# Optimization experiments

Measured on AMD Instinct MI355X. Metric: run time of the kernel, lower is better.

## Reference

```python
import jax, jax.numpy as jnp
import numpy as np
from jax import lax

B, T, D, H, W = 2, 8, 64, 64, 64
E, HID = 4, 256


def _layernorm(x, g, b, eps=1e-5):
    m = x.mean(-1, keepdims=True)
    v = ((x - m) ** 2).mean(-1, keepdims=True)
    return (x - m) / jnp.sqrt(v + eps) * g + b


def _pscan(A, X, axis):
    # linear recurrence h_t = A_t * h_{t-1} + X_t via associative scan
    def comb(l, r):
        a1, x1 = l
        a2, x2 = r
        return a2 * a1, a2 * x1 + x2
    return lax.associative_scan(comb, (A, X), axis=axis)[1]


def setup_inputs() -> dict:
    key = jax.random.key(0)
    ks = jax.random.split(key, 32)
    r = lambda i, shape, s=1.0: jax.random.normal(ks[i], shape, jnp.float32) * s
    D2 = 2 * D
    return {
        'x_re': r(0, (B, T, D, H, W)), 'x_im': r(1, (B, T, D, H, W)),
        'dt': jax.random.uniform(ks[2], (T,), jnp.float32, 0.5, 1.0),
        'ln_s_g': jnp.ones(D2), 'ln_s_b': jnp.zeros(D2),
        'conv_w': r(3, (3, 3, D2, D2), 0.03), 'conv_b': jnp.zeros(D2),
        'mom_w': r(4, (D2, D2), 0.08), 'mom_b': jnp.zeros(D2),
        'adv_w': jnp.full((1,), 0.1, jnp.float32),
        'enc_re': r(5, (D, D), 0.1), 'enc_im': r(6, (D, D), 0.1),
        'dec_re': r(7, (D, D), 0.1), 'dec_im': r(8, (D, D), 0.1),
        'flux_a_re': r(9, (D,)), 'flux_a_im': r(10, (D,), 0.1),
        'fin_re': r(11, (D, D), 0.1), 'fin_im': r(12, (D, D), 0.1),
        'fproj_re': r(13, (D, D), 0.1), 'fproj_im': r(14, (D, D), 0.1),
        'gate_w': r(15, (D2, D), 0.1), 'gate_b': jnp.zeros(D),
        'lam_re': r(16, (D,)), 'lam_im': r(17, (D,), 0.1),
        'noise_re': r(18, (B, T, H, W, D)), 'noise_im': r(19, (B, T, H, W, D)),
        'e_scale': jnp.full((1,), 0.1, jnp.float32),
        'ln_t_g': jnp.ones(D2), 'ln_t_b': jnp.zeros(D2),
        'router_w': r(20, (D2, E), 0.1), 'router_b': jnp.zeros(E),
        'w1': r(21, (E, D2, HID), 0.08), 'b1': jnp.zeros((E, HID)),
        'w2': r(22, (E, HID, D2), 0.08), 'b2': jnp.zeros((E, D2)),
    }


def _forward(x_re, x_im, dt, ln_s_g, ln_s_b, conv_w, conv_b, mom_w, mom_b, adv_w,
             enc_re, enc_im, dec_re, dec_im, flux_a_re, flux_a_im, fin_re, fin_im,
             fproj_re, fproj_im, gate_w, gate_b, lam_re, lam_im, noise_re, noise_im,
             e_scale, ln_t_g, ln_t_b, router_w, router_b, w1, b1, w2, b2):
    x = (x_re + 1j * x_im).astype(jnp.complex64)            # [B,T,D,H,W]
    target_energy = (jnp.abs(x) ** 2).mean(axis=(-2, -1))   # [B,T,D]
    momentum = x.mean(axis=(-2, -1))                        # [B,T,D] complex
    xcl = jnp.transpose(x, (0, 1, 3, 4, 2))                 # [B,T,H,W,D]
    Bs, Ts, Hs, Ws, Ds = xcl.shape
    D2 = 2 * Ds
    # --- spatial complex (Clifford) conv branch: LN over 2D channels + conv ---
    xr = jnp.concatenate([xcl.real, xcl.imag], -1)          # [B,T,H,W,2D]
    xn = _layernorm(xr, ln_s_g, ln_s_b)
    y = lax.conv_general_dilated(xn.reshape(Bs * Ts, Hs, Ws, D2), conv_w,
                                 (1, 1), 'SAME',
                                 dimension_numbers=('NHWC', 'HWIO', 'NHWC')) + conv_b
    y = y.reshape(Bs, Ts, Hs, Ws, D2)
    xcl = xcl + (y[..., :Ds] + 1j * y[..., Ds:])
    # --- momentum advection ---
    z_mean = xcl.mean(axis=(2, 3))                          # [B,T,D]
    mom_cat = jnp.concatenate([momentum.real, momentum.imag], -1) @ mom_w + mom_b
    mom_new = mom_cat[..., :Ds] + 1j * mom_cat[..., Ds:]
    dtb = jnp.broadcast_to(dt[None, :], (Bs, Ts))
    xcl = xcl + (mom_new * adv_w[0])[:, :, None, None, :] * dtb[:, :, None, None, None]
    momentum = 0.9 * momentum + 0.1 * z_mean
    # --- eigenbasis encode ---
    x_eigen = xcl @ (enc_re + 1j * enc_im)                  # [B,T,H,W,D]
    x_mean = x_eigen.mean(axis=(2, 3))                      # [B,T,D]
    # --- flux tracker: parallel scan over T ---
    A_flux = jnp.exp(-jax.nn.softplus(flux_a_re) + 1j * flux_a_im)
    A_flux = jnp.broadcast_to(A_flux, (Bs, Ts, Ds)).astype(jnp.complex64)
    X_flux = x_mean @ (fin_re + 1j * fin_im)
    flux_seq = _pscan(A_flux, X_flux, axis=1)               # [B,T,D]
    source = flux_seq @ (fproj_re + 1j * fproj_im)
    gate = jax.nn.sigmoid(jnp.concatenate([flux_seq.real, flux_seq.imag], -1) @ gate_w + gate_b)
    g = gate[:, :, None, None, :]
    forcing = x_eigen * g + source[:, :, None, None, :] * (1.0 - g)
    # --- temporal propagation: per-site parallel scan over T ---
    lam = -jax.nn.softplus(lam_re) + 1j * lam_im            # [D]
    op_decay = jnp.exp(lam[None, None, :] * dtb[:, :, None])  # [B,T,D]
    op_forcing = (op_decay - 1.0) / lam
    u_t = forcing * op_forcing[:, :, None, None, :]
    A_time = jnp.broadcast_to(op_decay[:, :, None, None, :], u_t.shape)
    u_out = _pscan(A_time, u_t, axis=1)                     # [B,T,H,W,D]
    noise = 0.01 * jnp.sqrt(dtb)[:, :, None, None, None] * (noise_re + 1j * noise_im)
    u_out = u_out + noise
    # --- decode + energy projection ---
    x_out = u_out @ (dec_re + 1j * dec_im)                  # [B,T,H,W,D]
    cur_e = (jnp.abs(x_out) ** 2).mean(axis=(2, 3))
    ratio = jnp.clip(target_energy / (cur_e + 1e-8), 0.5, 2.0)
    sf = jnp.sqrt(ratio)[:, :, None, None, :]
    x_out = x_out * (1.0 + e_scale[0] * (sf - 1.0))
    # --- temporal LN + MoE FFN on real-concat tokens ---
    xr2 = jnp.concatenate([x_out.real, x_out.imag], -1)
    xn2 = _layernorm(xr2, ln_t_g, ln_t_b)                   # [B,T,H,W,2D]
    tok = xn2.reshape(-1, D2)                               # [N,2D]
    p = jax.nn.softmax(tok @ router_w + router_b, -1)       # [N,E]
    hmid = jax.nn.gelu(jnp.einsum('nd,edh->neh', tok, w1) + b1)
    eout = jnp.einsum('neh,ehd->ned', hmid, w2) + b2
    out_tok = tok + jnp.einsum('ne,ned->nd', p, eout)
    out = out_tok.reshape(Bs, Ts, Hs, Ws, D2)
    x_out_c = out[..., :Ds] + 1j * out[..., Ds:]
    z_out = xcl + x_out_c
    z = jnp.transpose(z_out, (0, 1, 4, 2, 3))               # [B,T,D,H,W]
    return jnp.stack([z.real, z.imag])                      # [2,B,T,D,H,W]


def reference(x_re, x_im, dt, ln_s_g, ln_s_b, conv_w, conv_b, mom_w, mom_b, adv_w,
              enc_re, enc_im, dec_re, dec_im, flux_a_re, flux_a_im, fin_re, fin_im,
              fproj_re, fproj_im, gate_w, gate_b, lam_re, lam_im, noise_re, noise_im,
              e_scale, ln_t_g, ln_t_b, router_w, router_b, w1, b1, w2, b2):
    return _forward(x_re, x_im, dt, ln_s_g, ln_s_b, conv_w, conv_b, mom_w, mom_b, adv_w,
                    enc_re, enc_im, dec_re, dec_im, flux_a_re, flux_a_im, fin_re, fin_im,
                    fproj_re, fproj_im, gate_w, gate_b, lam_re, lam_im, noise_re, noise_im,
                    e_scale, ln_t_g, ln_t_b, router_w, router_b, w1, b1, w2, b2)
```

## Files before the change

### kernel.cpp

```cpp
#include <hip/hip_runtime.h>
#include <hip/hip_bf16.h>
#include <math.h>


#define W_C      8388608u
#define W_CWT    12582912u
#define W_W1T    14680064u
#define W_W2T    14745600u
#define W_ENCM   14811136u
#define W_DECM   14819328u
#define W_XMP_RE 14827520u
#define W_XMP_IM 14893056u
#define W_EP_RE  14958592u
#define W_EP_IM  15220736u
#define W_EIG_RE 16777216u
#define W_K1R    20971520u
#define W_K1I    21037056u
#define W_K1E    21102592u
#define W_SMALL  25165824u
#define W_TE     (W_SMALL+0u)
#define W_MTRE   (W_SMALL+3072u)
#define W_MTIM   (W_SMALL+4096u)
#define W_GATE   (W_SMALL+5120u)
#define W_SRCRE  (W_SMALL+6144u)
#define W_SRCIM  (W_SMALL+7168u)
#define W_OPFRE  (W_SMALL+8192u)
#define W_OPFIM  (W_SMALL+9216u)
#define W_OPDRE  (W_SMALL+10240u)
#define W_OPDIM  (W_SMALL+11264u)
#define W_SCALE  (W_SMALL+12288u)

#define XB_IM 4194304u

typedef __attribute__((ext_vector_type(8))) short bf16x8;
typedef __attribute__((ext_vector_type(4))) float f32x4;

__device__ __forceinline__ unsigned short bfr(float x) {
  __hip_bfloat16 h = __float2bfloat16(x);
  return *(unsigned short*)&h;
}
__device__ __forceinline__ unsigned int pk2(float a, float b) {
  return ((unsigned int)bfr(b) << 16) | (unsigned int)bfr(a);
}
__device__ __forceinline__ float sb2f(short s) {
  return __uint_as_float(((unsigned int)(unsigned short)s) << 16);
}

__global__ __launch_bounds__(256) void k2_transpose_ln(
    const float* __restrict__ xre, const float* __restrict__ xim,
    const float* __restrict__ g, const float* __restrict__ bb_, float* ws) {
  int blk = blockIdx.x; int bt = blk >> 6, h = blk & 63;
  __shared__ float tre[64][65], tim[64][65];
  __shared__ float ps[4][64], pq[4][64], pe[4][64];
  __shared__ float mean_l[64], rstd_l[64];
  size_t inbase = (size_t)bt * 262144 + (size_t)h * 64;
  for (int i = threadIdx.x; i < 1024; i += 256) {
    int d = i >> 4, w4 = (i & 15) * 4;
    float4 vr = *(const float4*)&xre[inbase + (size_t)d * 4096 + w4];
    float4 vi = *(const float4*)&xim[inbase + (size_t)d * 4096 + w4];
    tre[d][w4] = vr.x; tre[d][w4 + 1] = vr.y; tre[d][w4 + 2] = vr.z; tre[d][w4 + 3] = vr.w;
    tim[d][w4] = vi.x; tim[d][w4 + 1] = vi.y; tim[d][w4 + 2] = vi.z; tim[d][w4 + 3] = vi.w;
  }
  __syncthreads();
  {
    int w = threadIdx.x & 63, part = threadIdx.x >> 6;
    float s = 0.f, sq = 0.f;
    for (int dd = part * 16; dd < part * 16 + 16; dd++) {
      float vr = tre[dd][w], vi = tim[dd][w];
      s += vr + vi; sq += vr * vr + vi * vi;
    }
    ps[part][w] = s; pq[part][w] = sq;
  }
  __syncthreads();
  if (threadIdx.x < 64) {
    int w = threadIdx.x;
    float s  = ps[0][w] + ps[1][w] + ps[2][w] + ps[3][w];
    float sq = pq[0][w] + pq[1][w] + pq[2][w] + pq[3][w];
    float m = s / 128.f;
    float v = sq / 128.f - m * m;
    mean_l[w] = m; rstd_l[w] = rsqrtf(v + 1e-5f);
  }
  __syncthreads();
  {
    int d = threadIdx.x & 63, part = threadIdx.x >> 6;
    float sr = 0.f, si = 0.f, se = 0.f;
    for (int w = part * 16; w < part * 16 + 16; w++) {
      float vr = tre[d][w], vi = tim[d][w];
      sr += vr; si += vi; se += vr * vr + vi * vi;
    }
    ps[part][d] = sr; pq[part][d] = si; pe[part][d] = se;
  }
  __syncthreads();
  if (threadIdx.x < 64) {
    int d = threadIdx.x;
    int idx = h * 1024 + bt * 64 + d;
    ws[W_K1R + idx] = ps[0][d] + ps[1][d] + ps[2][d] + ps[3][d];
    ws[W_K1I + idx] = pq[0][d] + pq[1][d] + pq[2][d] + pq[3][d];
    ws[W_K1E + idx] = pe[0][d] + pe[1][d] + pe[2][d] + pe[3][d];
  }
  size_t tokbase = (size_t)blk * 64;
  __hip_bfloat16* xnb = (__hip_bfloat16*)(ws + W_C);
  int c0 = (threadIdx.x & 63) * 2, wg = threadIdx.x >> 6;
  float gc0 = g[c0], bc0 = bb_[c0], gc1 = g[c0 + 1], bc1 = bb_[c0 + 1];
  for (int pass = 0; pass < 16; pass++) {
    int w = pass * 4 + wg;
    float m = mean_l[w], rs = rstd_l[w];
    float v0 = (c0 < 64) ? tre[c0][w] : tim[c0 - 64][w];
    float v1 = (c0 + 1 < 64) ? tre[c0 + 1][w] : tim[c0 + 1 - 64][w];
    *(unsigned int*)&xnb[tokbase * 128 + (size_t)w * 128 + c0] =
        pk2((v0 - m) * rs * gc0 + bc0, (v1 - m) * rs * gc1 + bc1);
  }
}

__global__ void k1b2b(const float* __restrict__ mom_w, const float* __restrict__ mom_b,
                      const float* __restrict__ adv_w, const float* __restrict__ dt, float* ws) {
  int bt = blockIdx.x; int t = bt & 7;
  __shared__ float mc[128], outl[128];
  int tid = threadIdx.x;
  if (tid < 64) {
    int d = tid;
    float a = 0.f, b = 0.f, c = 0.f;
    for (int h = 0; h < 64; h++) {
      int idx = h * 1024 + bt * 64 + d;
      a += ws[W_K1R + idx]; b += ws[W_K1I + idx]; c += ws[W_K1E + idx];
    }
    ws[W_TE + bt * 64 + d] = c / 4096.f;
    mc[d] = a / 4096.f;
    mc[64 + d] = b / 4096.f;
  }
  __syncthreads();
  float acc = mom_b[tid];
  for (int k = 0; k < 128; k++) acc += mc[k] * mom_w[k * 128 + tid];
  outl[tid] = acc;
  __syncthreads();
  if (tid < 64) {
    float f = adv_w[0] * dt[t];
    ws[W_MTRE + bt * 64 + tid] = outl[tid] * f;
    ws[W_MTIM + bt * 64 + tid] = outl[64 + tid] * f;
  }
}

__global__ void k0_wprep(const float* __restrict__ w1, const float* __restrict__ w2,
                         const float* __restrict__ cw,
                         const float* __restrict__ enc_re, const float* __restrict__ enc_im,
                         const float* __restrict__ dec_re, const float* __restrict__ dec_im,
                         float* ws) {
  __hip_bfloat16* w1f = (__hip_bfloat16*)(ws + W_W1T);
  __hip_bfloat16* w2f = (__hip_bfloat16*)(ws + W_W2T);
  __hip_bfloat16* cwt = (__hip_bfloat16*)(ws + W_CWT);
  __hip_bfloat16* encM = (__hip_bfloat16*)(ws + W_ENCM);
  __hip_bfloat16* decM = (__hip_bfloat16*)(ws + W_DECM);
  int idx = blockIdx.x * 256 + threadIdx.x;
  if (idx < 131072) {
    {
      int j = idx & 7, lane = (idx >> 3) & 63, kt = (idx >> 9) & 3, nt = (idx >> 11) & 15, e = idx >> 15;
      int cout = nt * 16 + (lane & 15);
      int cin = kt * 32 + (lane >> 4) * 8 + j;
      w1f[idx] = __float2bfloat16(w1[((size_t)(e * 128 + cin)) * 256 + cout]);
    }
    {
      int j = idx & 7, lane = (idx >> 3) & 63, kt = (idx >> 9) & 7, nt = (idx >> 12) & 7, e = idx >> 15;
      int cout = nt * 16 + (lane & 15);
      int cin = kt * 32 + (lane >> 4) * 8 + j;
      w2f[idx] = __float2bfloat16(w2[((size_t)(e * 256 + cin)) * 128 + cout]);
    }
  }
  if (idx < 147456) {
    int j = idx & 7, lane = (idx >> 3) & 63, kt = (idx >> 9) & 3, r = idx >> 11;
    int nt = r & 7, tap = r >> 3;
    int cout = nt * 16 + (lane & 15);
    int cin = kt * 32 + (lane >> 4) * 8 + j;
    cwt[idx] = __float2bfloat16(cw[((size_t)(tap * 128 + cin)) * 128 + cout]);
  }
  if (idx < 16384) {
    int jj = idx & 7, lane = (idx >> 3) & 63, kt = (idx >> 9) & 3, nt = idx >> 11;
    int jc = nt * 16 + (lane & 15);
    int k = kt * 32 + (lane >> 4) * 8 + jj;
    float ve, vd;
    if (k < 64) {
      ve = (jc < 64) ? enc_re[k * 64 + jc] : enc_im[k * 64 + (jc - 64)];
      vd = (jc < 64) ? dec_re[k * 64 + jc] : dec_im[k * 64 + (jc - 64)];
    } else {
      int kk = k - 64;
      ve = (jc < 64) ? -enc_im[kk * 64 + jc] : enc_re[kk * 64 + (jc - 64)];
      vd = (jc < 64) ? -dec_im[kk * 64 + jc] : dec_re[kk * 64 + (jc - 64)];
    }
    encM[idx] = __float2bfloat16(ve);
    decM[idx] = __float2bfloat16(vd);
  }
}

__global__ __launch_bounds__(256) void k3_conv_enc(
    const float* __restrict__ xre, const float* __restrict__ xim,
    const float* __restrict__ cb, float* ws) {
  int blk = blockIdx.x; int bt = blk >> 6, h = blk & 63;
  const __hip_bfloat16* xnb = (const __hip_bfloat16*)(ws + W_C);
  const __hip_bfloat16* cwt = (const __hip_bfloat16*)(ws + W_CWT);
  const __hip_bfloat16* encM = (const __hip_bfloat16*)(ws + W_ENCM);
  __hip_bfloat16* xclb = (__hip_bfloat16*)ws;
  __hip_bfloat16* eigb = (__hip_bfloat16*)(ws + W_EIG_RE);
  __shared__ __align__(16) char smem[3 * 66 * 136 * 2];
  __hip_bfloat16 (*xin)[66][136] = (__hip_bfloat16(*)[66][136])smem;
  char* A = smem;
  int tid = threadIdx.x, lane = tid & 63, wv = tid >> 6;
  int arow = lane & 15, kgrp = (lane >> 4) * 8, rbase = (lane >> 4) * 4;

  for (int r = 0; r < 3; r++) {
    int hh = h + r - 1;
    if (hh < 0 || hh >= 64) {
      unsigned int* z = (unsigned int*)&xin[r][0][0];
      for (int i = tid; i < 4488; i += 256) z[i] = 0u;
    } else {
      if (tid < 68) *(unsigned int*)&xin[r][0][tid * 2] = 0u;
      else if (tid < 136) *(unsigned int*)&xin[r][65][(tid - 136 + 68) * 2] = 0u;
      const __hip_bfloat16* src = xnb + ((size_t)bt * 4096 + (size_t)hh * 64) * 128;
      for (int i = tid; i < 1024; i += 256) {
        int wp = (i >> 4) + 1, c8 = (i & 15) * 8;
        *(bf16x8*)&xin[r][wp][c8] = *(const bf16x8*)&src[(size_t)(wp - 1) * 128 + c8];
      }
    }
  }
  __syncthreads();

  f32x4 oacc[4][2];
  #pragma unroll
  for (int m = 0; m < 4; m++) {
    oacc[m][0] = (f32x4){0.f, 0.f, 0.f, 0.f};
    oacc[m][1] = (f32x4){0.f, 0.f, 0.f, 0.f};
  }

  for (int tap = 0; tap < 9; tap++) {
    int kh = tap / 3, kw = tap % 3;
    const __hip_bfloat16* wt0 = cwt + ((size_t)(tap * 8 + wv * 2) * 4) * 512 + lane * 8;
    #pragma unroll
    for (int kt = 0; kt < 4; kt++) {
      bf16x8 a[4];
      #pragma unroll
      for (int m = 0; m < 4; m++)
        a[m] = *(const bf16x8*)&xin[kh][m * 16 + arow + kw][kt * 32 + kgrp];
      bf16x8 b0 = *(const bf16x8*)&wt0[(size_t)kt * 512];
      bf16x8 b1 = *(const bf16x8*)&wt0[(size_t)(kt + 4) * 512];
      #pragma unroll
      for (int m = 0; m < 4; m++) {
        oacc[m][0] = __builtin_amdgcn_mfma_f32_16x16x32_bf16(a[m], b0, oacc[m][0], 0, 0, 0);
        oacc[m][1] = __builtin_amdgcn_mfma_f32_16x16x32_bf16(a[m], b1, oacc[m][1], 0, 0, 0);
      }
    }
  }
  __syncthreads();

  size_t rowtok = (size_t)blk * 64;
  #pragma unroll
  for (int n = 0; n < 2; n++) {
    int cout = (wv * 2 + n) * 16 + arow;
    bool isre = cout < 64;
    int d = cout & 63;
    float add = cb[cout] + ws[(isre ? W_MTRE : W_MTIM) + bt * 64 + d];
    size_t xb = isre ? 0u : XB_IM;
    const float* xsrc = (isre ? xre : xim) + ((size_t)(bt * 64 + d) * 64 + h) * 64;
    #pragma unroll
    for (int m = 0; m < 4; m++) {
      float4 xv = *(const float4*)&xsrc[m * 16 + rbase];
      #pragma unroll
      for (int r = 0; r < 4; r++) {
        int w = m * 16 + rbase + r;
        float xo = (r == 0) ? xv.x : (r == 1) ? xv.y : (r == 2) ? xv.z : xv.w;
        float v = xo + oacc[m][n][r] + add;
        xclb[xb + (rowtok + w) * 64 + d] = __float2bfloat16(v);
        *(__hip_bfloat16*)(A + w * 256 + ((cout * 2) ^ ((w & 7) << 4))) = __float2bfloat16(v);
      }
    }
  }
  __syncthreads();

  f32x4 acc[4][2];
  #pragma unroll
  for (int m = 0; m < 4; m++) {
    acc[m][0] = (f32x4){0.f, 0.f, 0.f, 0.f};
    acc[m][1] = (f32x4){0.f, 0.f, 0.f, 0.f};
  }
  #pragma unroll
  for (int kt = 0; kt < 4; kt++) {
    bf16x8 a[4];
    #pragma unroll
    for (int m = 0; m < 4; m++)
      a[m] = *(const bf16x8*)(A + (m * 16 + arow) * 256 + (((kt * 32 + kgrp) * 2) ^ ((arow & 7) << 4)));
    bf16x8 b0 = *(const bf16x8*)&encM[(((size_t)(wv * 2 + 0) * 4 + kt) * 64 + lane) * 8];
    bf16x8 b1 = *(const bf16x8*)&encM[(((size_t)(wv * 2 + 1) * 4 + kt) * 64 + lane) * 8];
    #pragma unroll
    for (int m = 0; m < 4; m++) {
      acc[m][0] = __builtin_amdgcn_mfma_f32_16x16x32_bf16(a[m], b0, acc[m][0], 0, 0, 0);
      acc[m][1] = __builtin_amdgcn_mfma_f32_16x16x32_bf16(a[m], b1, acc[m][1], 0, 0, 0);
    }
  }
  #pragma unroll
  for (int n = 0; n < 2; n++) {
    int jc = (wv * 2 + n) * 16 + arow;
    size_t eb = (jc < 64) ? 0u : XB_IM;
    int col = jc & 63;
    #pragma unroll
    for (int m = 0; m < 4; m++)
      #pragma unroll
      for (int r = 0; r < 4; r++)
        eigb[eb + (rowtok + m * 16 + rbase + r) * 64 + col] = __float2bfloat16(acc[m][n][r]);
    float s = 0.f;
    #pragma unroll
    for (int m = 0; m < 4; m++)
      #pragma unroll
      for (int r = 0; r < 4; r++) s += acc[m][n][r];
    s += __shfl_xor(s, 16);
    s += __shfl_xor(s, 32);
    if (lane < 16)
      ws[(jc < 64 ? W_XMP_RE : W_XMP_IM) + (size_t)blk * 64 + col] = s;
  }
}

__device__ __forceinline__ float softplusf(float x) {
  return (x > 20.f) ? x : log1pf(expf(x));
}

__global__ void k6_seq(const float* __restrict__ fin_re, const float* __restrict__ fin_im,
                       const float* __restrict__ fproj_re, const float* __restrict__ fproj_im,
                       const float* __restrict__ flux_a_re, const float* __restrict__ flux_a_im,
                       const float* __restrict__ gate_w, const float* __restrict__ gate_b,
                       const float* __restrict__ lam_re, const float* __restrict__ lam_im,
                       const float* __restrict__ dt, float* ws) {
  __shared__ float xmr[1024], xmi[1024], Xfr[1024], Xfi[1024], flr[1024], fli[1024];
  int tid = threadIdx.x;
  for (int i = tid; i < 1024; i += 256) {
    int bt = i >> 6, j = i & 63;
    float sr = 0.f, si = 0.f;
    for (int q = 0; q < 64; q++) {
      sr += ws[W_XMP_RE + (size_t)(bt * 64 + q) * 64 + j];
      si += ws[W_XMP_IM + (size_t)(bt * 64 + q) * 64 + j];
    }
    xmr[i] = sr / 4096.f; xmi[i] = si / 4096.f;
  }
  __syncthreads();
  for (int i = tid; i < 1024; i += 256) {
    int bt = i >> 6, j = i & 63;
    float ar = 0.f, ai = 0.f;
    for (int d = 0; d < 64; d++) {
      float xr = xmr[bt * 64 + d], xi = xmi[bt * 64 + d];
      float wr = fin_re[d * 64 + j], wi = fin_im[d * 64 + j];
      ar += xr * wr - xi * wi; ai += xr * wi + xi * wr;
    }
    Xfr[i] = ar; Xfi[i] = ai;
  }
  __syncthreads();
  if (tid < 128) {
    int b = tid >> 6, j = tid & 63;
    float mag = expf(-softplusf(flux_a_re[j]));
    float aar = mag * cosf(flux_a_im[j]), aai = mag * sinf(flux_a_im[j]);
    float sr = 0.f, si = 0.f;
    for (int t = 0; t < 8; t++) {
      int idx = (b * 8 + t) * 64 + j;
      float nr = aar * sr - aai * si + Xfr[idx];
      float ni = aar * si + aai * sr + Xfi[idx];
      sr = nr; si = ni;
      flr[idx] = sr; fli[idx] = si;
    }
  }
  __syncthreads();
  for (int i = tid; i < 1024; i += 256) {
    int bt = i >> 6, j = i & 63;
    float ar = 0.f, ai = 0.f, lg = 0.f;
    for (int d = 0; d < 64; d++) {
      float fr = flr[bt * 64 + d], fi = fli[bt * 64 + d];
      float wr = fproj_re[d * 64 + j], wi = fproj_im[d * 64 + j];
      ar += fr * wr - fi * wi; ai += fr * wi + fi * wr;
      lg += fr * gate_w[d * 64 + j] + fi * gate_w[(64 + d) * 64 + j];
    }
    ws[W_SRCRE + i] = ar; ws[W_SRCIM + i] = ai;
    ws[W_GATE + i] = 1.f / (1.f + expf(-(lg + gate_b[j])));
  }
  for (int i = tid; i < 1024; i += 256) {
    int bt = i >> 6, d = i & 63, t = bt & 7;
    float lr = -softplusf(lam_re[d]), li = lam_im[d];
    float dtv = dt[t];
    float mag = expf(lr * dtv);
    float dr = mag * cosf(li * dtv), di = mag * sinf(li * dtv);
    ws[W_OPDRE + i] = dr; ws[W_OPDIM + i] = di;
    float omr = dr - 1.f, omi = di;
    float den = lr * lr + li * li;
    ws[W_OPFRE + i] = (omr * lr + omi * li) / den;
    ws[W_OPFIM + i] = (omi * lr - omr * li) / den;
  }
}

__global__ __launch_bounds__(256) void k7_dec(const float* __restrict__ nre,
                                              const float* __restrict__ nim,
                                              const float* __restrict__ dt, float* ws) {
  int blk = blockIdx.x;
  int b = blk >> 8, h = (blk >> 2) & 63, wq = blk & 3;
  const __hip_bfloat16* decM = (const __hip_bfloat16*)(ws + W_DECM);
  __hip_bfloat16* eigb = (__hip_bfloat16*)(ws + W_EIG_RE);
  __shared__ float gl[8][64], srl[8][64], sil[8][64], ofr[8][64], ofi[8][64], odr[8][64], odi[8][64];
  __shared__ __align__(16) char A[2][4096];
  __shared__ float dts[8];
  int tid = threadIdx.x, lane = tid & 63, wv = tid >> 6;
  int arow = lane & 15, kgrp = (lane >> 4) * 8, rbase = (lane >> 4) * 4;
  for (int i = tid; i < 512; i += 256) {
    int t = i >> 6, d = i & 63, idx = (b * 8 + t) * 64 + d;
    gl[t][d]  = ws[W_GATE + idx];
    srl[t][d] = ws[W_SRCRE + idx]; sil[t][d] = ws[W_SRCIM + idx];
    ofr[t][d] = ws[W_OPFRE + idx]; ofi[t][d] = ws[W_OPFIM + idx];
    odr[t][d] = ws[W_OPDRE + idx]; odi[t][d] = ws[W_OPDIM + idx];
  }
  if (tid < 8) dts[tid] = dt[tid];
  __syncthreads();

  int dp = (tid & 31) * 2, wslot = tid >> 5;
  float ur[2][2], ui[2][2];
  #pragma unroll
  for (int a_ = 0; a_ < 2; a_++) { ur[a_][0] = 0.f; ur[a_][1] = 0.f; ui[a_][0] = 0.f; ui[a_][1] = 0.f; }

  for (int t = 0; t < 8; t++) {
    float ns = 0.01f * sqrtf(dts[t]);
    size_t tokb = ((size_t)(b * 8 + t) * 64 + h) * 64 + (size_t)wq * 16;
    char* At = A[t & 1];
    float g0 = gl[t][dp],  g1 = gl[t][dp + 1];
    float s0 = srl[t][dp], s1 = srl[t][dp + 1];
    float q0 = sil[t][dp], q1 = sil[t][dp + 1];
    float f0 = ofr[t][dp], f1 = ofr[t][dp + 1];
    float e0 = ofi[t][dp], e1 = ofi[t][dp + 1];
    float r0 = odr[t][dp], r1 = odr[t][dp + 1];
    float o0 = odi[t][dp], o1 = odi[t][dp + 1];
    #pragma unroll
    for (int wi = 0; wi < 2; wi++) {
      int wl = wslot + wi * 8;
      size_t off = (tokb + wl) * 64 + dp;
      unsigned int re2 = *(const unsigned int*)&eigb[off];
      unsigned int im2 = *(const unsigned int*)&eigb[XB_IM + off];
      float2 nr2 = *(const float2*)&nre[off];
      float2 ni2 = *(const float2*)&nim[off];
      float uo0, vo0, uo1, vo1;
      {
        float er_ = __uint_as_float(re2 << 16);
        float ei_ = __uint_as_float(im2 << 16);
        float fre = er_ * g0 + s0 * (1.f - g0);
        float fim = ei_ * g0 + q0 * (1.f - g0);
        float utr = fre * f0 - fim * e0;
        float uti = fre * e0 + fim * f0;
        float nur = r0 * ur[wi][0] - o0 * ui[wi][0] + utr;
        float nui = r0 * ui[wi][0] + o0 * ur[wi][0] + uti;
        ur[wi][0] = nur; ui[wi][0] = nui;
        uo0 = nur + ns * nr2.x; vo0 = nui + ns * ni2.x;
      }
      {
        float er_ = __uint_as_float(re2 & 0xffff0000u);
        float ei_ = __uint_as_float(im2 & 0xffff0000u);
        float fre = er_ * g1 + s1 * (1.f - g1);
        float fim = ei_ * g1 + q1 * (1.f - g1);
        float utr = fre * f1 - fim * e1;
        float uti = fre * e1 + fim * f1;
        float nur = r1 * ur[wi][1] - o1 * ui[wi][1] + utr;
        float nui = r1 * ui[wi][1] + o1 * ur[wi][1] + uti;
        ur[wi][1] = nur; ui[wi][1] = nui;
        uo1 = nur + ns * nr2.y; vo1 = nui + ns * ni2.y;
      }
      int sw = (wl & 7) << 4;
      *(unsigned int*)(At + wl * 256 + ((dp * 2) ^ sw)) = pk2(uo0, uo1);
      *(unsigned int*)(At + wl * 256 + ((128 + dp * 2) ^ sw)) = pk2(vo0, vo1);
    }
    __syncthreads();
    f32x4 acc[2];
    acc[0] = (f32x4){0.f, 0.f, 0.f, 0.f};
    acc[1] = (f32x4){0.f, 0.f, 0.f, 0.f};
    #pragma unroll
    for (int kt = 0; kt < 4; kt++) {
      bf16x8 a0 = *(const bf16x8*)(At + arow * 256 + (((kt * 32 + kgrp) * 2) ^ ((arow & 7) << 4)));
      bf16x8 b0 = *(const bf16x8*)&decM[(((size_t)(wv * 2 + 0) * 4 + kt) * 64 + lane) * 8];
      bf16x8 b1 = *(const bf16x8*)&decM[(((size_t)(wv * 2 + 1) * 4 + kt) * 64 + lane) * 8];
      acc[0] = __builtin_amdgcn_mfma_f32_16x16x32_bf16(a0, b0, acc[0], 0, 0, 0);
      acc[1] = __builtin_amdgcn_mfma_f32_16x16x32_bf16(a0, b1, acc[1], 0, 0, 0);
    }
    #pragma unroll
    for (int n = 0; n < 2; n++) {
      int jc = (wv * 2 + n) * 16 + arow;
      size_t eb = (jc < 64) ? 0u : XB_IM;
      int col = jc & 63;
      #pragma unroll
      for (int r = 0; r < 4; r++)
        eigb[eb + (tokb + rbase + r) * 64 + col] = __float2bfloat16(acc[n][r]);
      float s = acc[n][0] * acc[n][0] + acc[n][1] * acc[n][1]
              + acc[n][2] * acc[n][2] + acc[n][3] * acc[n][3];
      s += __shfl_xor(s, 16);
      s += __shfl_xor(s, 32);
      if (lane < 16)
        ws[(jc < 64 ? W_EP_RE : W_EP_IM)
           + (size_t)((b * 8 + t) * 256 + h * 4 + wq) * 64 + col] = s;
    }
  }
}

__global__ void k9b_scale(const float* __restrict__ escale, float* ws) {
  int bt = blockIdx.x; int j = threadIdx.x;
  float s = 0.f;
  for (int q = 0; q < 256; q++) {
    size_t idx = (size_t)(bt * 256 + q) * 64 + j;
    s += ws[W_EP_RE + idx] + ws[W_EP_IM + idx];
  }
  float cur = s / 4096.f;
  float te = ws[W_TE + bt * 64 + j];
  float ratio = te / (cur + 1e-8f);
  ratio = fminf(fmaxf(ratio, 0.5f), 2.0f);
  ws[W_SCALE + bt * 64 + j] = 1.f + escale[0] * (sqrtf(ratio) - 1.f);
}

__global__ __launch_bounds__(512) void k11_moe(
    const float* __restrict__ rw, const float* __restrict__ rb,
    const float* __restrict__ b1, const float* __restrict__ b2,
    const float* __restrict__ g2, const float* __restrict__ b2_,
    float* __restrict__ ws, float* __restrict__ out) {
  int blk = blockIdx.x; int bt = blk >> 6, h = blk & 63;
  const __hip_bfloat16* w1f = (const __hip_bfloat16*)(ws + W_W1T);
  const __hip_bfloat16* w2f = (const __hip_bfloat16*)(ws + W_W2T);
  const __hip_bfloat16* xclb = (const __hip_bfloat16*)ws;
  const __hip_bfloat16* eigb = (const __hip_bfloat16*)(ws + W_EIG_RE);
  __shared__ __align__(16) char smem[49152];
  __shared__ float pl[64][4];
  __shared__ float sc[64];
  __shared__ float mean_l[64], rstd_l[64];
  char* lt = smem;
  char* hb = smem + 16384;
  float (*obuf)[129] = (float(*)[129])smem;
  float* psq = (float*)(smem + 16384);
  int tid = threadIdx.x, lane = tid & 63, wv = tid >> 6;
  int arow = lane & 15, kgrp = (lane >> 4) * 8, rbase = (lane >> 4) * 4;
  size_t tokbase = (size_t)blk * 64;

  if (tid < 64) sc[tid] = ws[W_SCALE + bt * 64 + tid];
  __syncthreads();

  int w = tid >> 3, part = tid & 7;
  int c0 = part * 16, dbase = (part & 3) * 16;
  const __hip_bfloat16* rp = eigb + ((part < 4) ? 0u : XB_IM) + (tokbase + w) * 64 + dbase;
  float4 vv[4];
  {
    bf16x8 h0 = *(const bf16x8*)rp;
    bf16x8 h1 = *(const bf16x8*)(rp + 8);
    float f[16];
    #pragma unroll
    for (int j = 0; j < 8; j++) { f[j] = sb2f(h0[j]); f[8 + j] = sb2f(h1[j]); }
    float s = 0.f, sq = 0.f;
    #pragma unroll
    for (int q = 0; q < 4; q++) {
      float4 t4;
      t4.x = f[q * 4 + 0] * sc[dbase + q * 4 + 0];
      t4.y = f[q * 4 + 1] * sc[dbase + q * 4 + 1];
      t4.z = f[q * 4 + 2] * sc[dbase + q * 4 + 2];
      t4.w = f[q * 4 + 3] * sc[dbase + q * 4 + 3];
      vv[q] = t4;
      s  += t4.x + t4.y + t4.z + t4.w;
      sq += t4.x * t4.x + t4.y * t4.y + t4.z * t4.z + t4.w * t4.w;
    }
    psq[part * 64 + w] = s;
    psq[512 + part * 64 + w] = sq;
  }
  __syncthreads();
  if (tid < 64) {
    float s = 0.f, sq = 0.f;
    #pragma unroll
    for (int p = 0; p < 8; p++) { s += psq[p * 64 + tid]; sq += psq[512 + p * 64 + tid]; }
    float m = s / 128.f, v = sq / 128.f - m * m;
    mean_l[tid] = m; rstd_l[tid] = rsqrtf(v + 1e-5f);
  }
  __syncthreads();
  {
    float m = mean_l[w], rs = rstd_l[w];
    int szw = (w & 7) << 4;
    #pragma unroll
    for (int q = 0; q < 4; q++) {
      int c = c0 + q * 4;
      float a0 = (vv[q].x - m) * rs * g2[c]     + b2_[c];
      float a1 = (vv[q].y - m) * rs * g2[c + 1] + b2_[c + 1];
      float a2 = (vv[q].z - m) * rs * g2[c + 2] + b2_[c + 2];
      float a3 = (vv[q].w - m) * rs * g2[c + 3] + b2_[c + 3];
      *(unsigned int*)(lt + w * 256 + ((c * 2) ^ szw)) = pk2(a0, a1);
      *(unsigned int*)(lt + w * 256 + (((c + 2) * 2) ^ szw)) = pk2(a2, a3);
    }
  }
  __syncthreads();
  if (tid < 256) {
    int l = tid >> 2, e = tid & 3;
    float acc = rb[e];
    const float* rwe = rw + e;
    int sz = (l & 7) << 4;
    for (int dd = 0; dd < 128; dd += 2) {
      unsigned int u = *(const unsigned int*)(lt + l * 256 + ((dd * 2) ^ sz));
      float x0 = __uint_as_float(u << 16);
      float x1 = __uint_as_float(u & 0xffff0000u);
      acc += x0 * rwe[dd * 4] + x1 * rwe[dd * 4 + 4];
    }
    pl[l][e] = acc;
  }
  __syncthreads();
  if (tid < 64) {
    float m = fmaxf(fmaxf(pl[tid][0], pl[tid][1]), fmaxf(pl[tid][2], pl[tid][3]));
    float e0 = expf(pl[tid][0] - m), e1 = expf(pl[tid][1] - m);
    float e2 = expf(pl[tid][2] - m), e3 = expf(pl[tid][3] - m);
    float s = e0 + e1 + e2 + e3;
    float rs = __builtin_amdgcn_rcpf(s);
    pl[tid][0] = e0 * rs; pl[tid][1] = e1 * rs; pl[tid][2] = e2 * rs; pl[tid][3] = e3 * rs;
  }

  f32x4 oacc[4];
  #pragma unroll
  for (int m = 0; m < 4; m++) {
    int col = wv * 16 + arow;
    oacc[m] = (f32x4){0.f, 0.f, 0.f, 0.f};
    #pragma unroll
    for (int r = 0; r < 4; r++) {
      int row = m * 16 + rbase + r;
      oacc[m][r] = __bfloat162float(
          *(const __hip_bfloat16*)(lt + row * 256 + ((col * 2) ^ ((row & 7) << 4))));
    }
  }
  __syncthreads();

  for (int e = 0; e < 4; e++) {
    f32x4 acc1[4][2];
    #pragma unroll
    for (int m = 0; m < 4; m++) {
      acc1[m][0] = (f32x4){0.f, 0.f, 0.f, 0.f};
      acc1[m][1] = (f32x4){0.f, 0.f, 0.f, 0.f};
    }
    #pragma unroll
    for (int kt = 0; kt < 4; kt++) {
      bf16x8 a[4];
      #pragma unroll
      for (int m = 0; m < 4; m++) {
        int row = m * 16 + arow;
        a[m] = *(const bf16x8*)(lt + row * 256 + (((kt * 32 + kgrp) * 2) ^ ((arow & 7) << 4)));
      }
      bf16x8 b0 = *(const bf16x8*)&w1f[(((size_t)(e * 16 + wv * 2 + 0) * 4 + kt) * 64 + lane) * 8];
      bf16x8 b1 = *(const bf16x8*)&w1f[(((size_t)(e * 16 + wv * 2 + 1) * 4 + kt) * 64 + lane) * 8];
      #pragma unroll
      for (int m = 0; m < 4; m++) {
        acc1[m][0] = __builtin_amdgcn_mfma_f32_16x16x32_bf16(a[m], b0, acc1[m][0], 0, 0, 0);
        acc1[m][1] = __builtin_amdgcn_mfma_f32_16x16x32_bf16(a[m], b1, acc1[m][1], 0, 0, 0);
      }
    }
    __syncthreads();
    #pragma unroll
    for (int n = 0; n < 2; n++) {
      int col = (wv * 2 + n) * 16 + arow;
      float bv = b1[e * 256 + col];
      #pragma unroll
      for (int m = 0; m < 4; m++)
        #pragma unroll
        for (int r = 0; r < 4; r++) {
          float hv = acc1[m][n][r] + bv;
          float z = 1.5957691216f * hv + 0.0713548162f * hv * hv * hv;
          float gelu = hv * __builtin_amdgcn_rcpf(1.f + __expf(-z));
          int row = m * 16 + rbase + r;
          *(__hip_bfloat16*)(hb + row * 512 + ((col * 2) ^ ((row & 7) << 4))) =
              __float2bfloat16(gelu);
        }
    }
    __syncthreads();
    f32x4 acc2[4];
    #pragma unroll
    for (int m = 0; m < 4; m++) acc2[m] = (f32x4){0.f, 0.f, 0.f, 0.f};
    #pragma unroll
    for (int kt = 0; kt < 8; kt++) {
      bf16x8 a2[4];
      #pragma unroll
      for (int m = 0; m < 4; m++) {
        int row = m * 16 + arow;
        a2[m] = *(const bf16x8*)(hb + row * 512 + (((kt * 32 + kgrp) * 2) ^ ((arow & 7) << 4)));
      }
      bf16x8 bb = *(const bf16x8*)&w2f[(((size_t)(e * 8 + wv) * 8 + kt) * 64 + lane) * 8];
      #pragma unroll
      for (int m = 0; m < 4; m++)
        acc2[m] = __builtin_amdgcn_mfma_f32_16x16x32_bf16(a2[m], bb, acc2[m], 0, 0, 0);
    }
    {
      int col = wv * 16 + arow;
      float bv2 = b2[e * 128 + col];
      #pragma unroll
      for (int m = 0; m < 4; m++)
        #pragma unroll
        for (int r = 0; r < 4; r++)
          oacc[m][r] += pl[m * 16 + rbase + r][e] * (acc2[m][r] + bv2);
    }
  }

  __syncthreads();
  #pragma unroll
  for (int m = 0; m < 4; m++) {
    int col = wv * 16 + arow;
    #pragma unroll
    for (int r = 0; r < 4; r++)
      obuf[m * 16 + rbase + r][col] = oacc[m][r];
  }
  __syncthreads();

  for (int i = tid; i < 4096; i += 512) {
    int wt = i >> 6, c0r = (i & 63) * 2;
    size_t xb = (c0r < 64) ? 0u : XB_IM;
    int dd = c0r & 63;
    unsigned int u = *(const unsigned int*)&xclb[xb + (tokbase + wt) * 64 + dd];
    obuf[wt][c0r]     += __uint_as_float(u << 16);
    obuf[wt][c0r + 1] += __uint_as_float(u & 0xffff0000u);
  }
  __syncthreads();
  for (int i = tid; i < 8192; i += 512) {
    int d2 = i >> 6, wt = i & 63;
    out[(size_t)(d2 >> 6) * 4194304 + (size_t)bt * 262144 + (size_t)(d2 & 63) * 4096
        + (size_t)h * 64 + wt] = obuf[wt][d2];
  }
}

extern "C" void kernel_launch(void* const* d_in, const int* in_sizes, int n_in,
                              void* d_out, int out_size, void* d_ws, size_t ws_size,
                              hipStream_t stream) {
  const float* x_re      = (const float*)d_in[0];
  const float* x_im      = (const float*)d_in[1];
  const float* dt        = (const float*)d_in[2];
  const float* ln_s_g    = (const float*)d_in[3];
  const float* ln_s_b    = (const float*)d_in[4];
  const float* conv_w    = (const float*)d_in[5];
  const float* conv_b    = (const float*)d_in[6];
  const float* mom_w     = (const float*)d_in[7];
  const float* mom_b     = (const float*)d_in[8];
  const float* adv_w     = (const float*)d_in[9];
  const float* enc_re    = (const float*)d_in[10];
  const float* enc_im    = (const float*)d_in[11];
  const float* dec_re    = (const float*)d_in[12];
  const float* dec_im    = (const float*)d_in[13];
  const float* flux_a_re = (const float*)d_in[14];
  const float* flux_a_im = (const float*)d_in[15];
  const float* fin_re    = (const float*)d_in[16];
  const float* fin_im    = (const float*)d_in[17];
  const float* fproj_re  = (const float*)d_in[18];
  const float* fproj_im  = (const float*)d_in[19];
  const float* gate_w    = (const float*)d_in[20];
  const float* gate_b    = (const float*)d_in[21];
  const float* lam_re    = (const float*)d_in[22];
  const float* lam_im    = (const float*)d_in[23];
  const float* noise_re  = (const float*)d_in[24];
  const float* noise_im  = (const float*)d_in[25];
  const float* e_scale   = (const float*)d_in[26];
  const float* ln_t_g    = (const float*)d_in[27];
  const float* ln_t_b    = (const float*)d_in[28];
  const float* router_w  = (const float*)d_in[29];
  const float* router_b  = (const float*)d_in[30];
  const float* w1        = (const float*)d_in[31];
  const float* b1        = (const float*)d_in[32];
  const float* w2        = (const float*)d_in[33];
  const float* b2        = (const float*)d_in[34];
  float* ws  = (float*)d_ws;
  float* out = (float*)d_out;

  k0_wprep<<<576, 256, 0, stream>>>(w1, w2, conv_w, enc_re, enc_im, dec_re, dec_im, ws);
  k2_transpose_ln<<<1024, 256, 0, stream>>>(x_re, x_im, ln_s_g, ln_s_b, ws);
  k1b2b<<<16, 128, 0, stream>>>(mom_w, mom_b, adv_w, dt, ws);
  k3_conv_enc<<<1024, 256, 0, stream>>>(x_re, x_im, conv_b, ws);
  k6_seq<<<1, 256, 0, stream>>>(fin_re, fin_im, fproj_re, fproj_im, flux_a_re, flux_a_im,
                                gate_w, gate_b, lam_re, lam_im, dt, ws);
  k7_dec<<<512, 256, 0, stream>>>(noise_re, noise_im, dt, ws);
  k9b_scale<<<16, 64, 0, stream>>>(e_scale, ws);
  k11_moe<<<1024, 512, 0, stream>>>(router_w, router_b, b1, b2, ln_t_g, ln_t_b, ws, out);
}
```

Measured before the change: 253.1 us.

## Split MoE kernel into 32-token blocks with 4-wave 2x4 MFMA tiling

The fused MoE kernel now processes 32 tokens per block with 256 threads instead of 64 tokens with 512 threads, doubling the grid to 2048 blocks. Each wave now computes a 2x4 (first GEMM) and 2x2 (second GEMM) tile of 16x16 MFMA outputs, reusing each loaded A fragment across more N tiles. Shared memory per block halves, which allows more resident blocks and better occupancy. The trade-off is that each block reloads the expert weights for only half as many tokens, doubling total weight traffic from L2.

New measurement: 255.7 us. No clear change (+1.0%).

```diff
diff --git a/kernel.cpp b/kernel.cpp
--- a/kernel.cpp
+++ b/kernel.cpp
@@ -508,27 +508,28 @@
   ws[W_SCALE + bt * 64 + j] = 1.f + escale[0] * (sqrtf(ratio) - 1.f);
 }
 
-__global__ __launch_bounds__(512) void k11_moe(
+__global__ __launch_bounds__(256) void k11_moe(
     const float* __restrict__ rw, const float* __restrict__ rb,
     const float* __restrict__ b1, const float* __restrict__ b2,
     const float* __restrict__ g2, const float* __restrict__ b2_,
     float* __restrict__ ws, float* __restrict__ out) {
-  int blk = blockIdx.x; int bt = blk >> 6, h = blk & 63;
+  int blk = blockIdx.x;
+  int bt = blk >> 7, h = (blk >> 1) & 63, w0 = (blk & 1) * 32;
   const __hip_bfloat16* w1f = (const __hip_bfloat16*)(ws + W_W1T);
   const __hip_bfloat16* w2f = (const __hip_bfloat16*)(ws + W_W2T);
   const __hip_bfloat16* xclb = (const __hip_bfloat16*)ws;
   const __hip_bfloat16* eigb = (const __hip_bfloat16*)(ws + W_EIG_RE);
-  __shared__ __align__(16) char smem[49152];
-  __shared__ float pl[64][4];
+  __shared__ __align__(16) char smem[24576];
+  __shared__ float pl[32][4];
   __shared__ float sc[64];
-  __shared__ float mean_l[64], rstd_l[64];
+  __shared__ float mean_l[32], rstd_l[32];
   char* lt = smem;
-  char* hb = smem + 16384;
+  char* hb = smem + 8192;
   float (*obuf)[129] = (float(*)[129])smem;
-  float* psq = (float*)(smem + 16384);
+  float* psq = (float*)(smem + 8192);
   int tid = threadIdx.x, lane = tid & 63, wv = tid >> 6;
   int arow = lane & 15, kgrp = (lane >> 4) * 8, rbase = (lane >> 4) * 4;
-  size_t tokbase = (size_t)blk * 64;
+  size_t tokbase = (size_t)blk * 32;
 
   if (tid < 64) sc[tid] = ws[W_SCALE + bt * 64 + tid];
   __syncthreads();
@@ -555,14 +556,14 @@
       s  += t4.x + t4.y + t4.z + t4.w;
       sq += t4.x * t4.x + t4.y * t4.y + t4.z * t4.z + t4.w * t4.w;
     }
-    psq[part * 64 + w] = s;
-    psq[512 + part * 64 + w] = sq;
-  }
-  __syncthreads();
-  if (tid < 64) {
+    psq[part * 32 + w] = s;
+    psq[256 + part * 32 + w] = sq;
+  }
+  __syncthreads();
+  if (tid < 32) {
     float s = 0.f, sq = 0.f;
     #pragma unroll
-    for (int p = 0; p < 8; p++) { s += psq[p * 64 + tid]; sq += psq[512 + p * 64 + tid]; }
+    for (int p = 0; p < 8; p++) { s += psq[p * 32 + tid]; sq += psq[256 + p * 32 + tid]; }
     float m = s / 128.f, v = sq / 128.f - m * m;
     mean_l[tid] = m; rstd_l[tid] = rsqrtf(v + 1e-5f);
   }
@@ -582,7 +583,7 @@
     }
   }
   __syncthreads();
-  if (tid < 256) {
+  if (tid < 128) {
     int l = tid >> 2, e = tid & 3;
     float acc = rb[e];
     const float* rwe = rw + e;
@@ -596,7 +597,7 @@
     pl[l][e] = acc;
   }
   __syncthreads();
-  if (tid < 64) {
+  if (tid < 32) {
     float m = fmaxf(fmaxf(pl[tid][0], pl[tid][1]), fmaxf(pl[tid][2], pl[tid][3]));
     float e0 = expf(pl[tid][0] - m), e1 = expf(pl[tid][1] - m);
     float e2 = expf(pl[tid][2] - m), e3 = expf(pl[tid][3] - m);
@@ -605,50 +606,51 @@
     pl[tid][0] = e0 * rs; pl[tid][1] = e1 * rs; pl[tid][2] = e2 * rs; pl[tid][3] = e3 * rs;
   }
 
-  f32x4 oacc[4];
+  f32x4 oacc[2][2];
   #pragma unroll
-  for (int m = 0; m < 4; m++) {
-    int col = wv * 16 + arow;
-    oacc[m] = (f32x4){0.f, 0.f, 0.f, 0.f};
-    #pragma unroll
-    for (int r = 0; r < 4; r++) {
-      int row = m * 16 + rbase + r;
-      oacc[m][r] = __bfloat162float(
-          *(const __hip_bfloat16*)(lt + row * 256 + ((col * 2) ^ ((row & 7) << 4))));
-    }
-  }
+  for (int m = 0; m < 2; m++)
+    #pragma unroll
+    for (int n = 0; n < 2; n++) {
+      int col = (wv * 2 + n) * 16 + arow;
+      oacc[m][n] = (f32x4){0.f, 0.f, 0.f, 0.f};
+      #pragma unroll
+      for (int r = 0; r < 4; r++) {
+        int row = m * 16 + rbase + r;
+        oacc[m][n][r] = __bfloat162float(
+            *(const __hip_bfloat16*)(lt + row * 256 + ((col * 2) ^ ((row & 7) << 4))));
+      }
+    }
   __syncthreads();
 
   for (int e = 0; e < 4; e++) {
-    f32x4 acc1[4][2];
-    #pragma unroll
-    for (int m = 0; m < 4; m++) {
-      acc1[m][0] = (f32x4){0.f, 0.f, 0.f, 0.f};
-      acc1[m][1] = (f32x4){0.f, 0.f, 0.f, 0.f};
-    }
+    f32x4 acc1[2][4];
+    #pragma unroll
+    for (int m = 0; m < 2; m++)
+      #pragma unroll
+      for (int n = 0; n < 4; n++) acc1[m][n] = (f32x4){0.f, 0.f, 0.f, 0.f};
     #pragma unroll
     for (int kt = 0; kt < 4; kt++) {
-      bf16x8 a[4];
-      #pragma unroll
-      for (int m = 0; m < 4; m++) {
+      bf16x8 a[2];
+      #pragma unroll
+      for (int m = 0; m < 2; m++) {
         int row = m * 16 + arow;
         a[m] = *(const bf16x8*)(lt + row * 256 + (((kt * 32 + kgrp) * 2) ^ ((arow & 7) << 4)));
       }
-      bf16x8 b0 = *(const bf16x8*)&w1f[(((size_t)(e * 16 + wv * 2 + 0) * 4 + kt) * 64 + lane) * 8];
-      bf16x8 b1 = *(const bf16x8*)&w1f[(((size_t)(e * 16 + wv * 2 + 1) * 4 + kt) * 64 + lane) * 8];
-      #pragma unroll
-      for (int m = 0; m < 4; m++) {
-        acc1[m][0] = __builtin_amdgcn_mfma_f32_16x16x32_bf16(a[m], b0, acc1[m][0], 0, 0, 0);
-        acc1[m][1] = __builtin_amdgcn_mfma_f32_16x16x32_bf16(a[m], b1, acc1[m][1], 0, 0, 0);
+      #pragma unroll
+      for (int n = 0; n < 4; n++) {
+        bf16x8 bb = *(const bf16x8*)&w1f[(((size_t)(e * 16 + wv * 4 + n) * 4 + kt) * 64 + lane) * 8];
+        #pragma unroll
+        for (int m = 0; m < 2; m++)
+          acc1[m][n] = __builtin_amdgcn_mfma_f32_16x16x32_bf16(a[m], bb, acc1[m][n], 0, 0, 0);
       }
     }
     __syncthreads();
     #pragma unroll
-    for (int n = 0; n < 2; n++) {
-      int col = (wv * 2 + n) * 16 + arow;
+    for (int n = 0; n < 4; n++) {
+      int col = (wv * 4 + n) * 16 + arow;
       float bv = b1[e * 256 + col];
       #pragma unroll
-      for (int m = 0; m < 4; m++)
+      for (int m = 0; m < 2; m++)
         #pragma unroll
         for (int r = 0; r < 4; r++) {
           float hv = acc1[m][n][r] + bv;
@@ -660,44 +662,53 @@
         }
     }
     __syncthreads();
-    f32x4 acc2[4];
-    #pragma unroll
-    for (int m = 0; m < 4; m++) acc2[m] = (f32x4){0.f, 0.f, 0.f, 0.f};
+    f32x4 acc2[2][2];
+    #pragma unroll
+    for (int m = 0; m < 2; m++) {
+      acc2[m][0] = (f32x4){0.f, 0.f, 0.f, 0.f};
+      acc2[m][1] = (f32x4){0.f, 0.f, 0.f, 0.f};
+    }
     #pragma unroll
     for (int kt = 0; kt < 8; kt++) {
-      bf16x8 a2[4];
-      #pragma unroll
-      for (int m = 0; m < 4; m++) {
+      bf16x8 a2[2];
+      #pragma unroll
+      for (int m = 0; m < 2; m++) {
         int row = m * 16 + arow;
         a2[m] = *(const bf16x8*)(hb + row * 512 + (((kt * 32 + kgrp) * 2) ^ ((arow & 7) << 4)));
       }
-      bf16x8 bb = *(const bf16x8*)&w2f[(((size_t)(e * 8 + wv) * 8 + kt) * 64 + lane) * 8];
-      #pragma unroll
-      for (int m = 0; m < 4; m++)
-        acc2[m] = __builtin_amdgcn_mfma_f32_16x16x32_bf16(a2[m], bb, acc2[m], 0, 0, 0);
-    }
-    {
-      int col = wv * 16 + arow;
+      bf16x8 bb0 = *(const bf16x8*)&w2f[(((size_t)(e * 8 + wv * 2 + 0) * 8 + kt) * 64 + lane) * 8];
+      bf16x8 bb1 = *(const bf16x8*)&w2f[(((size_t)(e * 8 + wv * 2 + 1) * 8 + kt) * 64 + lane) * 8];
+      #pragma unroll
+      for (int m = 0; m < 2; m++) {
+        acc2[m][0] = __builtin_amdgcn_mfma_f32_16x16x32_bf16(a2[m], bb0, acc2[m][0], 0, 0, 0);
+        acc2[m][1] = __builtin_amdgcn_mfma_f32_16x16x32_bf16(a2[m], bb1, acc2[m][1], 0, 0, 0);
+      }
+    }
+    #pragma unroll
+    for (int n = 0; n < 2; n++) {
+      int col = (wv * 2 + n) * 16 + arow;
       float bv2 = b2[e * 128 + col];
       #pragma unroll
-      for (int m = 0; m < 4; m++)
+      for (int m = 0; m < 2; m++)
         #pragma unroll
         for (int r = 0; r < 4; r++)
-          oacc[m][r] += pl[m * 16 + rbase + r][e] * (acc2[m][r] + bv2);
+          oacc[m][n][r] += pl[m * 16 + rbase + r][e] * (acc2[m][n][r] + bv2);
     }
   }
 
   __syncthreads();
   #pragma unroll
-  for (int m = 0; m < 4; m++) {
-    int col = wv * 16 + arow;
-    #pragma unroll
-    for (int r = 0; r < 4; r++)
-      obuf[m * 16 + rbase + r][col] = oacc[m][r];
-  }
-  __syncthreads();
-
-  for (int i = tid; i < 4096; i += 512) {
+  for (int m = 0; m < 2; m++)
+    #pragma unroll
+    for (int n = 0; n < 2; n++) {
+      int col = (wv * 2 + n) * 16 + arow;
+      #pragma unroll
+      for (int r = 0; r < 4; r++)
+        obuf[m * 16 + rbase + r][col] = oacc[m][n][r];
+    }
+  __syncthreads();
+
+  for (int i = tid; i < 2048; i += 256) {
     int wt = i >> 6, c0r = (i & 63) * 2;
     size_t xb = (c0r < 64) ? 0u : XB_IM;
     int dd = c0r & 63;
@@ -706,10 +717,10 @@
     obuf[wt][c0r + 1] += __uint_as_float(u & 0xffff0000u);
   }
   __syncthreads();
-  for (int i = tid; i < 8192; i += 512) {
-    int d2 = i >> 6, wt = i & 63;
+  for (int i = tid; i < 4096; i += 256) {
+    int d2 = i >> 5, wt = i & 31;
     out[(size_t)(d2 >> 6) * 4194304 + (size_t)bt * 262144 + (size_t)(d2 & 63) * 4096
-        + (size_t)h * 64 + wt] = obuf[wt][d2];
+        + (size_t)h * 64 + w0 + wt] = obuf[wt][d2];
   }
 }
 
@@ -762,5 +773,5 @@
                                 gate_w, gate_b, lam_re, lam_im, dt, ws);
   k7_dec<<<512, 256, 0, stream>>>(noise_re, noise_im, dt, ws);
   k9b_scale<<<16, 64, 0, stream>>>(e_scale, ws);
-  k11_moe<<<1024, 512, 0, stream>>>(router_w, router_b, b1, b2, ln_t_g, ln_t_b, ws, out);
-}
+  k11_moe<<<2048, 256, 0, stream>>>(router_w, router_b, b1, b2, ln_t_g, ln_t_b, ws, out);
+}
```
